# Kernel tuning notes

Measured on AMD Instinct MI355X. Metric: run time of the kernel, lower is better.

The kernel has to match this reference:

```python
import jax, jax.numpy as jnp
import numpy as np

N = 200000; B = 4; C3D = 64; C2D = 128; H = 96; W = 312; MID = 128; OUT = 128
EPS = 1e-5


def _bn(x, g, b):
    # BatchNorm1d in training mode: batch stats over point dim, biased var
    m = x.mean(0, keepdims=True)
    v = x.var(0, keepdims=True)
    return (x - m) * jax.lax.rsqrt(v + EPS) * g + b


def setup_inputs() -> dict:
    key = jax.random.key(0)
    ks = jax.random.split(key, 16)
    bidx = jnp.sort(jax.random.randint(ks[0], (N,), 0, B))  # sorted batch ids (matches per-batch concat order)
    z = jax.random.randint(ks[1], (N,), 0, 40)
    y = jax.random.randint(ks[2], (N,), 0, 1600)
    x = jax.random.randint(ks[3], (N,), 0, 1408)
    voxel_coords = jnp.stack([bidx, z, y, x], 1).astype(jnp.int32)
    voxel_features = jax.random.normal(ks[4], (N, C3D), jnp.float32)
    image_features = jax.random.normal(ks[5], (B, C2D, H, W), jnp.float32)
    base = np.array([[180.0, 0.0, W / 2.0, 0.0],
                     [0.0, 180.0, H / 2.0, 0.0],
                     [0.0, 0.0, 1.0, 0.0]], np.float32)
    P2 = jnp.asarray(base)[None] + 0.01 * jax.random.normal(ks[6], (B, 3, 4), jnp.float32)
    s = 0.05
    params = {
        'vt_w1': s * jax.random.normal(ks[7], (MID, C3D), jnp.float32),
        'vt_b1': jnp.zeros((MID,), jnp.float32),
        'bn1_g': jnp.ones((MID,), jnp.float32),
        'bn1_b': jnp.zeros((MID,), jnp.float32),
        'vt_w2': s * jax.random.normal(ks[8], (MID, MID), jnp.float32),
        'vt_b2': jnp.zeros((MID,), jnp.float32),
        'att_w1': s * jax.random.normal(ks[9], (MID, 2 * MID), jnp.float32),
        'att_b1': jnp.zeros((MID,), jnp.float32),
        'att_w2': s * jax.random.normal(ks[10], (1, MID), jnp.float32),
        'att_b2': jnp.zeros((1,), jnp.float32),
        'fus_w': s * jax.random.normal(ks[11], (OUT, 2 * MID), jnp.float32),
        'fus_b': jnp.zeros((OUT,), jnp.float32),
        'bnf_g': jnp.ones((OUT,), jnp.float32),
        'bnf_b': jnp.zeros((OUT,), jnp.float32),
    }
    return {'voxel_features': voxel_features, 'voxel_coords': voxel_coords,
            'image_features': image_features, 'P2': P2, **params}


def _forward(voxel_features, voxel_coords, image_features, P2,
             vt_w1, vt_b1, bn1_g, bn1_b, vt_w2, vt_b2,
             att_w1, att_b1, att_w2, att_b2, fus_w, fus_b, bnf_g, bnf_b):
    # voxel transform: Linear -> BN -> ReLU -> Linear
    h = voxel_features @ vt_w1.T + vt_b1
    h = jax.nn.relu(_bn(h, bn1_g, bn1_b))
    vfeat = h @ vt_w2.T + vt_b2                                  # (N, MID)

    # 3D -> 2D projection (source multiplies [z,y,x] by voxel_size, faithfully kept)
    voxel_size = jnp.array([0.05, 0.05, 0.1], jnp.float32)
    pc_min = jnp.array([0.0, -40.0, -3.0], jnp.float32)
    pts = voxel_coords[:, 1:].astype(jnp.float32) * voxel_size + pc_min  # (N, 3)
    homo = jnp.concatenate([pts, jnp.ones((pts.shape[0], 1), jnp.float32)], 1)
    b = voxel_coords[:, 0]
    cam = jnp.einsum('nd,nkd->nk', homo, P2[b])                  # (N, 3)
    p2d = cam[:, :2] / (cam[:, 2:3] + 1e-8)
    gx = jnp.clip(p2d[:, 0] / W * 2 - 1, -1.0, 1.0)
    gy = jnp.clip(p2d[:, 1] / H * 2 - 1, -1.0, 1.0)

    # bilinear grid_sample, align_corners=False, zero padding
    ix = ((gx + 1) * W - 1) * 0.5
    iy = ((gy + 1) * H - 1) * 0.5
    x0f = jnp.floor(ix); y0f = jnp.floor(iy)
    wx1 = ix - x0f; wy1 = iy - y0f
    x0 = x0f.astype(jnp.int32); y0 = y0f.astype(jnp.int32)

    def corner(yc, xc, w):
        valid = (xc >= 0) & (xc < W) & (yc >= 0) & (yc < H)
        f = image_features[b, :, jnp.clip(yc, 0, H - 1), jnp.clip(xc, 0, W - 1)]  # (N, C2D)
        return f * (w * valid)[:, None]

    ifeat = (corner(y0, x0, (1 - wx1) * (1 - wy1))
             + corner(y0, x0 + 1, wx1 * (1 - wy1))
             + corner(y0 + 1, x0, (1 - wx1) * wy1)
             + corner(y0 + 1, x0 + 1, wx1 * wy1))                # (N, C2D)

    # attention gate + weighted fusion + Conv1d(k=1) -> BN -> ReLU
    comb = jnp.concatenate([vfeat, ifeat], 1)                    # (N, 2*MID)
    a = jax.nn.sigmoid(jax.nn.relu(comb @ att_w1.T + att_b1) @ att_w2.T + att_b2)  # (N, 1)
    fused = jnp.concatenate([vfeat * a, ifeat * (1 - a)], 1)     # (N, 2*MID)
    out = fused @ fus_w.T + fus_b                                # (N, OUT)
    return jax.nn.relu(_bn(out, bnf_g, bnf_b))


def reference(voxel_features, voxel_coords, image_features, P2,
              vt_w1, vt_b1, bn1_g, bn1_b, vt_w2, vt_b2,
              att_w1, att_b1, att_w2, att_b2, fus_w, fus_b, bnf_g, bnf_b):
    return _forward(voxel_features, voxel_coords, image_features, P2,
                    vt_w1, vt_b1, bn1_g, bn1_b, vt_w2, vt_b2,
                    att_w1, att_b1, att_w2, att_b2, fus_w, fus_b, bnf_g, bnf_b)
```

## Files before the change

### kernel.cpp

```cpp
#include <hip/hip_runtime.h>
#include <hip/hip_bf16.h>

#define NPTS 200000
#define BB   4
#define C3D  64
#define C2D  128
#define HH   96
#define WW   312
#define MID  128
#define OUTC 128

#define WB_W1   0
#define WB_W2   8192
#define WB_AW1  24576
#define WB_AW2  57344
#define WB_FW   57472
#define WB_TOTAL 90240

#define FXS 1048576.0f
#define FXI (1.0 / 1048576.0)

#define WS_H0S    45120
#define WS_H0Q    49216
#define WS_SUM64  53440
#define WS_SSQ64  57536
#define ZERO_N    16512
#define WS_DERIV  61632
#define WS_IMG    62144

typedef __attribute__((ext_vector_type(8))) short s16x8;
typedef __attribute__((ext_vector_type(4))) float f32x4;

__device__ __forceinline__ ushort f2bf(float f) {
    unsigned u = __float_as_uint(f);
    unsigned r = (u + 0x7FFFu + ((u >> 16) & 1u)) >> 16;
    return (ushort)r;
}
__device__ __forceinline__ float bf2f(ushort u) {
    return __uint_as_float(((unsigned)u) << 16);
}
__device__ __forceinline__ void atomic_fx(unsigned long long* p, float v) {
    atomicAdd(p, (unsigned long long)(long long)llrintf(v * FXS));
}
__device__ __forceinline__ s16x8 pack_bf8(float4 a, float4 b) {
    s16x8 v;
    v[0] = (short)f2bf(a.x); v[1] = (short)f2bf(a.y);
    v[2] = (short)f2bf(a.z); v[3] = (short)f2bf(a.w);
    v[4] = (short)f2bf(b.x); v[5] = (short)f2bf(b.y);
    v[6] = (short)f2bf(b.z); v[7] = (short)f2bf(b.w);
    return v;
}

__global__ __launch_bounds__(256) void k_transpose(const float* __restrict__ img,
                                                   ushort* __restrict__ img_bf,
                                                   float* __restrict__ stats,
                                                   const float* __restrict__ w1,
                                                   const float* __restrict__ w2,
                                                   const float* __restrict__ aw1,
                                                   const float* __restrict__ aw2,
                                                   const float* __restrict__ fw,
                                                   ushort* __restrict__ wb) {
    __shared__ float tile[32][33];
    int flat = blockIdx.x * 256 + threadIdx.x;
    if (flat < ZERO_N) stats[flat] = 0.f;
    if (flat < WB_TOTAL) {
        float v;
        if      (flat < WB_W2)  v = w1[flat - WB_W1];
        else if (flat < WB_AW1) v = w2[flat - WB_W2];
        else if (flat < WB_AW2) v = aw1[flat - WB_AW1];
        else if (flat < WB_FW)  v = aw2[flat - WB_AW2];
        else                    v = fw[flat - WB_FW];
        wb[flat] = f2bf(v);
    }

    int bid = blockIdx.x;
    int ct = bid & 3;  bid >>= 2;
    int wt = bid % 10; bid /= 10;
    int h  = bid % HH;
    int b  = bid / HH;
    int tx = threadIdx.x & 31, ty = threadIdx.x >> 5;
    int w0 = wt * 32, c0 = ct * 32;

    #pragma unroll
    for (int i = 0; i < 4; i++) {
        int c = c0 + ty + 8 * i;
        int w = w0 + tx;
        float v = 0.f;
        if (w < WW) v = img[((b * C2D + c) * HH + h) * WW + w];
        tile[ty + 8 * i][tx] = v;
    }
    __syncthreads();
    #pragma unroll
    for (int i = 0; i < 4; i++) {
        int w = w0 + ty + 8 * i;
        int c = c0 + tx;
        if (w < WW) img_bf[((b * HH + h) * WW + w) * C2D + c] = f2bf(tile[tx][ty + 8 * i]);
    }
}

#define H0_ROWS   320
#define H0_BLOCKS (NPTS / H0_ROWS)

__global__ __launch_bounds__(256) void k_h0stats(
        const float* __restrict__ x, const ushort* __restrict__ wb,
        unsigned long long* __restrict__ hs64,
        unsigned long long* __restrict__ hq64) {
    __shared__ float red[4][256];
    const ushort* w1b = wb + WB_W1;
    int t = threadIdx.x, lane = t & 63, wv = t >> 6;
    int l15 = lane & 15, lq = lane >> 4;
    float psum[8], pssq[8];
    #pragma unroll
    for (int nt = 0; nt < 8; nt++) { psum[nt] = 0.f; pssq[nt] = 0.f; }

    int r0 = blockIdx.x * H0_ROWS;
    #pragma unroll 1
    for (int ch = 0; ch < 5; ch++) {
        const float* xr = x + (long)(r0 + ch * 64 + wv * 16 + l15) * C3D;
        float4 xa0 = *(const float4*)(xr + lq * 8);
        float4 xa1 = *(const float4*)(xr + lq * 8 + 4);
        float4 xb0 = *(const float4*)(xr + 32 + lq * 8);
        float4 xb1 = *(const float4*)(xr + 32 + lq * 8 + 4);
        s16x8 af0 = pack_bf8(xa0, xa1);
        s16x8 af1 = pack_bf8(xb0, xb1);
        #pragma unroll
        for (int nt = 0; nt < 8; nt++) {
            f32x4 acc = {0.f, 0.f, 0.f, 0.f};
            s16x8 bf0 = *(const s16x8*)(w1b + (nt * 16 + l15) * 64 + lq * 8);
            s16x8 bf1 = *(const s16x8*)(w1b + (nt * 16 + l15) * 64 + 32 + lq * 8);
            acc = __builtin_amdgcn_mfma_f32_16x16x32_bf16(af0, bf0, acc, 0, 0, 0);
            acc = __builtin_amdgcn_mfma_f32_16x16x32_bf16(af1, bf1, acc, 0, 0, 0);
            psum[nt] += acc[0] + acc[1] + acc[2] + acc[3];
            pssq[nt] += acc[0]*acc[0] + acc[1]*acc[1] + acc[2]*acc[2] + acc[3]*acc[3];
        }
    }
    #pragma unroll
    for (int nt = 0; nt < 8; nt++) {
        psum[nt] += __shfl_xor(psum[nt], 16, 64);
        psum[nt] += __shfl_xor(psum[nt], 32, 64);
        pssq[nt] += __shfl_xor(pssq[nt], 16, 64);
        pssq[nt] += __shfl_xor(pssq[nt], 32, 64);
    }
    if (lane < 16) {
        #pragma unroll
        for (int nt = 0; nt < 8; nt++) {
            red[wv][nt * 16 + l15]       = psum[nt];
            red[wv][128 + nt * 16 + l15] = pssq[nt];
        }
    }
    __syncthreads();
    {
        float v = red[0][t] + red[1][t] + red[2][t] + red[3][t];
        int c = t & 127;
        int slot = blockIdx.x & 15;
        if (t < 128) atomic_fx(&hs64[c * 16 + slot], v);
        else         atomic_fx(&hq64[c * 16 + slot], v);
    }
}

__global__ void k_fin1(const unsigned long long* __restrict__ hs64,
                       const unsigned long long* __restrict__ hq64,
                       const float* __restrict__ g, const float* __restrict__ be,
                       float* __restrict__ s, float* __restrict__ sh) {
    int c = threadIdx.x;
    long long si = 0, qi = 0;
    #pragma unroll
    for (int i = 0; i < 16; i++) {
        si += (long long)hs64[c * 16 + i];
        qi += (long long)hq64[c * 16 + i];
    }
    float S = (float)((double)si * FXI);
    float Q = (float)((double)qi * FXI);
    const float invN = 1.f / (float)NPTS;
    float m = S * invN;
    float v = Q * invN - m * m;
    float sc = g[c] * rsqrtf(v + 1e-5f);
    s[c] = sc;
    sh[c] = be[c] - m * sc;
}

__global__ __launch_bounds__(256, 3) void k_main(
    const float* __restrict__ x, const int* __restrict__ coords,
    const ushort* __restrict__ img_bf, const float* __restrict__ P2,
    const ushort* __restrict__ wb,
    const float* __restrict__ bn1s, const float* __restrict__ bn1sh,
    const float* __restrict__ b2, const float* __restrict__ ab1,
    const float* __restrict__ ab2, const float* __restrict__ fb,
    float* __restrict__ out,
    unsigned long long* __restrict__ sum64, unsigned long long* __restrict__ ssq64)
{
    __shared__ __align__(16) char smem[34816];
    ushort* combs  = (ushort*)smem;
    float*  outs   = (float*)smem;
    float*  a_part = (float*)(smem + 33792);

    const ushort* w1b  = wb + WB_W1;
    const ushort* w2b  = wb + WB_W2;
    const ushort* aw1b = wb + WB_AW1;
    const ushort* aw2b = wb + WB_AW2;
    const ushort* fwb  = wb + WB_FW;

    int t = threadIdx.x;
    int n0 = blockIdx.x * 64;
    int lane = t & 63, wv = t >> 6;
    int l15 = lane & 15, lq = lane >> 4;
    int m0 = wv * 16;
    int cb = wv * 32;

    int grow = m0 + (lane >> 2);
    int qc = lane & 3;
    int poff_[4]; float pwgt_[4];
    {
        int4 cd = *(const int4*)(coords + (long)(n0 + grow) * 4);
        int b = cd.x;
        float p0 = (float)cd.y * 0.05f;
        float p1 = (float)cd.z * 0.05f - 40.f;
        float p2 = (float)cd.w * 0.1f - 3.f;
        const float* P = P2 + b * 12;
        float cam0 = P[0] * p0 + P[1] * p1 + P[2]  * p2 + P[3];
        float cam1 = P[4] * p0 + P[5] * p1 + P[6]  * p2 + P[7];
        float cam2 = P[8] * p0 + P[9] * p1 + P[10] * p2 + P[11];
        float d = cam2 + 1e-8f;
        float px = cam0 / d, py = cam1 / d;
        float gx = fminf(fmaxf(px / (float)WW * 2.f - 1.f, -1.f), 1.f);
        float gy = fminf(fmaxf(py / (float)HH * 2.f - 1.f, -1.f), 1.f);
        float ix = ((gx + 1.f) * (float)WW - 1.f) * 0.5f;
        float iy = ((gy + 1.f) * (float)HH - 1.f) * 0.5f;
        float x0f = floorf(ix), y0f = floorf(iy);
        float wx = ix - x0f, wy = iy - y0f;
        int x0 = (int)x0f, y0 = (int)y0f;
        #pragma unroll
        for (int j = 0; j < 4; j++) {
            int xc = x0 + (j & 1), yc = y0 + (j >> 1);
            float wgt = ((j & 1) ? wx : 1.f - wx) * ((j >> 1) ? wy : 1.f - wy);
            bool valid = (xc >= 0) && (xc < WW) && (yc >= 0) && (yc < HH);
            int xcc = min(max(xc, 0), WW - 1), ycc = min(max(yc, 0), HH - 1);
            poff_[j] = ((b * HH + ycc) * WW + xcc) * C2D;
            pwgt_[j] = valid ? wgt : 0.f;
        }
    }

    #pragma unroll
    for (int g = 0; g < 4; g++) {
        float a8[8];
        #pragma unroll
        for (int e = 0; e < 8; e++) a8[e] = 0.f;
        #pragma unroll
        for (int j = 0; j < 4; j++) {
            s16x8 v = *(const s16x8*)(img_bf + poff_[j] + qc * 32 + g * 8);
            float wgt = pwgt_[j];
            #pragma unroll
            for (int e = 0; e < 8; e++)
                a8[e] += wgt * bf2f((ushort)v[e]);
        }
        s16x8 o;
        #pragma unroll
        for (int e = 0; e < 8; e++) o[e] = (short)f2bf(a8[e]);
        *(s16x8*)(combs + grow * 264 + 128 + qc * 32 + g * 8) = o;
    }

    s16x8 af0, af1;
    {
        const float* xr = x + (long)(n0 + m0 + l15) * C3D;
        float4 xa0 = *(const float4*)(xr + lq * 8);
        float4 xa1 = *(const float4*)(xr + lq * 8 + 4);
        float4 xb0 = *(const float4*)(xr + 32 + lq * 8);
        float4 xb1 = *(const float4*)(xr + 32 + lq * 8 + 4);
        af0 = pack_bf8(xa0, xa1);
        af1 = pack_bf8(xb0, xb1);
    }

    #pragma unroll
    for (int nt = 0; nt < 8; nt++) {
        f32x4 acc = {0.f, 0.f, 0.f, 0.f};
        s16x8 bf0 = *(const s16x8*)(w1b + (nt * 16 + l15) * 64 + lq * 8);
        s16x8 bf1 = *(const s16x8*)(w1b + (nt * 16 + l15) * 64 + 32 + lq * 8);
        acc = __builtin_amdgcn_mfma_f32_16x16x32_bf16(af0, bf0, acc, 0, 0, 0);
        acc = __builtin_amdgcn_mfma_f32_16x16x32_bf16(af1, bf1, acc, 0, 0, 0);
        int c = nt * 16 + l15;
        float sc = bn1s[c], shf = bn1sh[c];
        #pragma unroll
        for (int r = 0; r < 4; r++)
            combs[(m0 + lq * 4 + r) * 264 + c] = f2bf(fmaxf(acc[r] * sc + shf, 0.f));
    }
    __syncthreads();

    f32x4 vacc[4][2];
    #pragma unroll
    for (int nt2 = 0; nt2 < 2; nt2++) {
        int c = cb + nt2 * 16 + l15;
        s16x8 wf[4];
        #pragma unroll
        for (int s = 0; s < 4; s++)
            wf[s] = *(const s16x8*)(w2b + c * 128 + s * 32 + lq * 8);
        #pragma unroll
        for (int mt = 0; mt < 4; mt++) {
            s16x8 ah[4];
            #pragma unroll
            for (int s = 0; s < 4; s++)
                ah[s] = *(const s16x8*)(combs + (mt * 16 + l15) * 264 + s * 32 + lq * 8);
            f32x4 acc = {0.f, 0.f, 0.f, 0.f};
            #pragma unroll
            for (int s = 0; s < 4; s++)
                acc = __builtin_amdgcn_mfma_f32_16x16x32_bf16(ah[s], wf[s], acc, 0, 0, 0);
            vacc[mt][nt2] = acc;
        }
    }
    __syncthreads();

    #pragma unroll
    for (int nt2 = 0; nt2 < 2; nt2++) {
        int c = cb + nt2 * 16 + l15;
        float bb = b2[c];
        #pragma unroll
        for (int mt = 0; mt < 4; mt++)
            #pragma unroll
            for (int r = 0; r < 4; r++)
                combs[(mt * 16 + lq * 4 + r) * 264 + c] = f2bf(vacc[mt][nt2][r] + bb);
    }
    __syncthreads();

    float sp[4][4];
    #pragma unroll
    for (int mt = 0; mt < 4; mt++)
        #pragma unroll
        for (int r = 0; r < 4; r++) sp[mt][r] = 0.f;
    #pragma unroll
    for (int nt2 = 0; nt2 < 2; nt2++) {
        int c = cb + nt2 * 16 + l15;
        s16x8 wf[8];
        #pragma unroll
        for (int s = 0; s < 8; s++)
            wf[s] = *(const s16x8*)(aw1b + c * 256 + s * 32 + lq * 8);
        float bb = ab1[c];
        float w2c = bf2f(aw2b[c]);
        #pragma unroll
        for (int mt = 0; mt < 4; mt++) {
            s16x8 afm[8];
            #pragma unroll
            for (int s = 0; s < 8; s++)
                afm[s] = *(const s16x8*)(combs + (mt * 16 + l15) * 264 + s * 32 + lq * 8);
            f32x4 acc = {0.f, 0.f, 0.f, 0.f};
            #pragma unroll
            for (int s = 0; s < 8; s++)
                acc = __builtin_amdgcn_mfma_f32_16x16x32_bf16(afm[s], wf[s], acc, 0, 0, 0);
            #pragma unroll
            for (int r = 0; r < 4; r++)
                sp[mt][r] += fmaxf(acc[r] + bb, 0.f) * w2c;
        }
    }
    #pragma unroll
    for (int d = 1; d < 16; d <<= 1) {
        #pragma unroll
        for (int mt = 0; mt < 4; mt++)
            #pragma unroll
            for (int r = 0; r < 4; r++)
                sp[mt][r] += __shfl_xor(sp[mt][r], d, 64);
    }
    if (l15 == 0) {
        #pragma unroll
        for (int mt = 0; mt < 4; mt++) {
            f32x4 v = {sp[mt][0], sp[mt][1], sp[mt][2], sp[mt][3]};
            *(f32x4*)(a_part + wv * 64 + mt * 16 + lq * 4) = v;
        }
    }
    __syncthreads();

    {
        int row = m0 + l15;
        float s0 = ab2[0] + a_part[row] + a_part[64 + row] + a_part[128 + row]
                 + a_part[192 + row];
        float a = 1.f / (1.f + expf(-s0));
        #pragma unroll
        for (int j = 0; j < 8; j++) {
            int ch = lq * 8 + j;
            float f = (ch < 16) ? a : 1.f - a;
            ushort* p = combs + row * 264 + ch * 8;
            s16x8 v = *(s16x8*)p;
            s16x8 o;
            #pragma unroll
            for (int e = 0; e < 8; e++) o[e] = (short)f2bf(bf2f((ushort)v[e]) * f);
            *(s16x8*)p = o;
        }
    }
    __syncthreads();

    f32x4 facc[4][2];
    #pragma unroll
    for (int nt2 = 0; nt2 < 2; nt2++) {
        int c = cb + nt2 * 16 + l15;
        s16x8 wf[8];
        #pragma unroll
        for (int s = 0; s < 8; s++)
            wf[s] = *(const s16x8*)(fwb + c * 256 + s * 32 + lq * 8);
        #pragma unroll
        for (int mt = 0; mt < 4; mt++) {
            s16x8 afm[8];
            #pragma unroll
            for (int s = 0; s < 8; s++)
                afm[s] = *(const s16x8*)(combs + (mt * 16 + l15) * 264 + s * 32 + lq * 8);
            f32x4 acc = {0.f, 0.f, 0.f, 0.f};
            #pragma unroll
            for (int s = 0; s < 8; s++)
                acc = __builtin_amdgcn_mfma_f32_16x16x32_bf16(afm[s], wf[s], acc, 0, 0, 0);
            facc[mt][nt2] = acc;
        }
    }
    __syncthreads();

    #pragma unroll
    for (int nt2 = 0; nt2 < 2; nt2++) {
        int c = cb + nt2 * 16 + l15;
        float bb = fb[c];
        #pragma unroll
        for (int mt = 0; mt < 4; mt++)
            #pragma unroll
            for (int r = 0; r < 4; r++)
                outs[(mt * 16 + lq * 4 + r) * 132 + c] = facc[mt][nt2][r] + bb;
    }
    __syncthreads();

    {
        float4* og = (float4*)(out + (long)n0 * OUTC);
        #pragma unroll
        for (int i = 0; i < 8; i++) {
            int f4 = t + 256 * i;
            int row = f4 >> 5, c4 = f4 & 31;
            float4 v = *(const float4*)(outs + row * 132 + c4 * 4);
            og[row * 32 + c4] = v;
        }
        int slot = blockIdx.x & 15;
        if (t < 128) {
            float S = 0.f;
            #pragma unroll 8
            for (int row = 0; row < 64; row++) S += outs[row * 132 + t];
            atomic_fx(&sum64[t * 16 + slot], S);
        } else {
            int c = t - 128;
            float Q = 0.f;
            #pragma unroll 8
            for (int row = 0; row < 64; row++) { float v = outs[row * 132 + c]; Q += v * v; }
            atomic_fx(&ssq64[c * 16 + slot], Q);
        }
    }
}

__global__ __launch_bounds__(256) void k_bnf(float* __restrict__ out,
                                             const unsigned long long* __restrict__ sum64,
                                             const unsigned long long* __restrict__ ssq64,
                                             const float* __restrict__ g,
                                             const float* __restrict__ b) {
    __shared__ float s_s[128], s_sh[128];
    int t = threadIdx.x;
    if (t < 128) {
        long long si = 0, qi = 0;
        #pragma unroll
        for (int i = 0; i < 16; i++) {
            si += (long long)sum64[t * 16 + i];
            qi += (long long)ssq64[t * 16 + i];
        }
        float S = (float)((double)si * FXI);
        float Q = (float)((double)qi * FXI);
        const float invN = 1.f / (float)NPTS;
        float m = S * invN;
        float v = Q * invN - m * m;
        float sc = g[t] * rsqrtf(v + 1e-5f);
        s_s[t] = sc;
        s_sh[t] = b[t] - m * sc;
    }
    __syncthreads();

    long i = (long)blockIdx.x * 256 + t;
    float4* p = (float4*)out;
    float4 v = p[i];
    int c4 = (int)(i & 31);
    float4 sv  = *(const float4*)(s_s + c4 * 4);
    float4 shv = *(const float4*)(s_sh + c4 * 4);
    v.x = fmaxf(v.x * sv.x + shv.x, 0.f);
    v.y = fmaxf(v.y * sv.y + shv.y, 0.f);
    v.z = fmaxf(v.z * sv.z + shv.z, 0.f);
    v.w = fmaxf(v.w * sv.w + shv.w, 0.f);
    p[i] = v;
}

extern "C" void kernel_launch(void* const* d_in, const int* in_sizes, int n_in,
                              void* d_out, int out_size, void* d_ws, size_t ws_size,
                              hipStream_t stream) {
    const float* x      = (const float*)d_in[0];
    const int*   coords = (const int*)d_in[1];
    const float* img    = (const float*)d_in[2];
    const float* P2     = (const float*)d_in[3];
    const float* w1     = (const float*)d_in[4];
    const float* b1     = (const float*)d_in[5];
    const float* g1     = (const float*)d_in[6];
    const float* be1    = (const float*)d_in[7];
    const float* w2     = (const float*)d_in[8];
    const float* b2     = (const float*)d_in[9];
    const float* aw1    = (const float*)d_in[10];
    const float* ab1    = (const float*)d_in[11];
    const float* aw2    = (const float*)d_in[12];
    const float* ab2    = (const float*)d_in[13];
    const float* fw     = (const float*)d_in[14];
    const float* fb     = (const float*)d_in[15];
    const float* gf     = (const float*)d_in[16];
    const float* bef    = (const float*)d_in[17];
    float* out = (float*)d_out;
    (void)b1;

    float* wsf = (float*)d_ws;
    ushort* wb = (ushort*)wsf;
    unsigned long long* hs64  = (unsigned long long*)(wsf + WS_H0S);
    unsigned long long* hq64  = (unsigned long long*)(wsf + WS_H0Q);
    unsigned long long* sum64 = (unsigned long long*)(wsf + WS_SUM64);
    unsigned long long* ssq64 = (unsigned long long*)(wsf + WS_SSQ64);
    float* zero_base = wsf + WS_H0S;
    float* s1  = wsf + WS_DERIV;
    float* sh1 = s1 + 128;
    ushort* img_bf = (ushort*)(wsf + WS_IMG);

    k_transpose<<<BB * HH * 10 * 4, 256, 0, stream>>>(img, img_bf, zero_base,
                                                      w1, w2, aw1, aw2, fw, wb);
    k_h0stats<<<H0_BLOCKS, 256, 0, stream>>>(x, wb, hs64, hq64);
    k_fin1<<<1, 128, 0, stream>>>(hs64, hq64, g1, be1, s1, sh1);
    k_main<<<NPTS / 64, 256, 0, stream>>>(x, coords, img_bf, P2, wb, s1, sh1,
                                          b2, ab1, ab2, fb, out, sum64, ssq64);
    k_bnf<<<NPTS * OUTC / 4 / 256, 256, 0, stream>>>(out, sum64, ssq64, gf, bef);
}
```

Baseline: 469.5 us.

## Merge transpose and BN1 stats kernels, fold finalize into main kernel

The image transpose/weight-conversion kernel and the first-layer BN statistics kernel become one launch by splitting the grid by block index. The stats branch converts w1 to bf16 itself from fp32, since it can no longer rely on the converted weights. The one-block finalize kernel is removed: every k_main block recomputes the BN1 scale and shift from the fixed-point accumulators into shared memory. Stats zeroing moves to a memset. This cuts two kernel launches and their serialization, at the cost of redundant per-block finalize work in k_main and an extra barrier.

```diff
diff --git a/kernel.cpp b/kernel.cpp
--- a/kernel.cpp
+++ b/kernel.cpp
@@ -24,8 +24,7 @@
 #define WS_H0Q    49216
 #define WS_SUM64  53440
 #define WS_SSQ64  57536
-#define ZERO_N    16512
-#define WS_DERIV  61632
+#define WS_STATS_END 61632
 #define WS_IMG    62144
 
 typedef __attribute__((ext_vector_type(8))) short s16x8;
@@ -51,18 +50,86 @@
     return v;
 }
 
-__global__ __launch_bounds__(256) void k_transpose(const float* __restrict__ img,
-                                                   ushort* __restrict__ img_bf,
-                                                   float* __restrict__ stats,
-                                                   const float* __restrict__ w1,
-                                                   const float* __restrict__ w2,
-                                                   const float* __restrict__ aw1,
-                                                   const float* __restrict__ aw2,
-                                                   const float* __restrict__ fw,
-                                                   ushort* __restrict__ wb) {
+#define TRANS_BLOCKS (BB * HH * 10 * 4)
+#define H0_ROWS   320
+#define H0_BLOCKS (NPTS / H0_ROWS)
+
+__global__ __launch_bounds__(256, 3) void k_pre(
+        const float* __restrict__ img, ushort* __restrict__ img_bf,
+        const float* __restrict__ w1, const float* __restrict__ w2,
+        const float* __restrict__ aw1, const float* __restrict__ aw2,
+        const float* __restrict__ fw, ushort* __restrict__ wb,
+        const float* __restrict__ x,
+        unsigned long long* __restrict__ hs64,
+        unsigned long long* __restrict__ hq64) {
     __shared__ float tile[32][33];
+    __shared__ float red[4][256];
+
+    if (blockIdx.x >= TRANS_BLOCKS) {
+        int hbid = blockIdx.x - TRANS_BLOCKS;
+        int t = threadIdx.x, lane = t & 63, wv = t >> 6;
+        int l15 = lane & 15, lq = lane >> 4;
+
+        s16x8 wfa[8], wfb[8];
+        #pragma unroll
+        for (int nt = 0; nt < 8; nt++) {
+            const float* wr = w1 + (nt * 16 + l15) * 64;
+            float4 a0 = *(const float4*)(wr + lq * 8);
+            float4 a1 = *(const float4*)(wr + lq * 8 + 4);
+            float4 b0 = *(const float4*)(wr + 32 + lq * 8);
+            float4 b1 = *(const float4*)(wr + 32 + lq * 8 + 4);
+            wfa[nt] = pack_bf8(a0, a1);
+            wfb[nt] = pack_bf8(b0, b1);
+        }
+        float psum[8], pssq[8];
+        #pragma unroll
+        for (int nt = 0; nt < 8; nt++) { psum[nt] = 0.f; pssq[nt] = 0.f; }
+
+        int r0 = hbid * H0_ROWS;
+        #pragma unroll 1
+        for (int ch = 0; ch < 5; ch++) {
+            const float* xr = x + (long)(r0 + ch * 64 + wv * 16 + l15) * C3D;
+            float4 xa0 = *(const float4*)(xr + lq * 8);
+            float4 xa1 = *(const float4*)(xr + lq * 8 + 4);
+            float4 xb0 = *(const float4*)(xr + 32 + lq * 8);
+            float4 xb1 = *(const float4*)(xr + 32 + lq * 8 + 4);
+            s16x8 af0 = pack_bf8(xa0, xa1);
+            s16x8 af1 = pack_bf8(xb0, xb1);
+            #pragma unroll
+            for (int nt = 0; nt < 8; nt++) {
+                f32x4 acc = {0.f, 0.f, 0.f, 0.f};
+                acc = __builtin_amdgcn_mfma_f32_16x16x32_bf16(af0, wfa[nt], acc, 0, 0, 0);
+                acc = __builtin_amdgcn_mfma_f32_16x16x32_bf16(af1, wfb[nt], acc, 0, 0, 0);
+                psum[nt] += acc[0] + acc[1] + acc[2] + acc[3];
+                pssq[nt] += acc[0]*acc[0] + acc[1]*acc[1] + acc[2]*acc[2] + acc[3]*acc[3];
+            }
+        }
+        #pragma unroll
+        for (int nt = 0; nt < 8; nt++) {
+            psum[nt] += __shfl_xor(psum[nt], 16, 64);
+            psum[nt] += __shfl_xor(psum[nt], 32, 64);
+            pssq[nt] += __shfl_xor(pssq[nt], 16, 64);
+            pssq[nt] += __shfl_xor(pssq[nt], 32, 64);
+        }
+        if (lane < 16) {
+            #pragma unroll
+            for (int nt = 0; nt < 8; nt++) {
+                red[wv][nt * 16 + l15]       = psum[nt];
+                red[wv][128 + nt * 16 + l15] = pssq[nt];
+            }
+        }
+        __syncthreads();
+        {
+            float v = red[0][t] + red[1][t] + red[2][t] + red[3][t];
+            int c = t & 127;
+            int slot = hbid & 15;
+            if (t < 128) atomic_fx(&hs64[c * 16 + slot], v);
+            else         atomic_fx(&hq64[c * 16 + slot], v);
+        }
+        return;
+    }
+
     int flat = blockIdx.x * 256 + threadIdx.x;
-    if (flat < ZERO_N) stats[flat] = 0.f;
     if (flat < WB_TOTAL) {
         float v;
         if      (flat < WB_W2)  v = w1[flat - WB_W1];
@@ -98,92 +165,13 @@
     }
 }
 
-#define H0_ROWS   320
-#define H0_BLOCKS (NPTS / H0_ROWS)
-
-__global__ __launch_bounds__(256) void k_h0stats(
-        const float* __restrict__ x, const ushort* __restrict__ wb,
-        unsigned long long* __restrict__ hs64,
-        unsigned long long* __restrict__ hq64) {
-    __shared__ float red[4][256];
-    const ushort* w1b = wb + WB_W1;
-    int t = threadIdx.x, lane = t & 63, wv = t >> 6;
-    int l15 = lane & 15, lq = lane >> 4;
-    float psum[8], pssq[8];
-    #pragma unroll
-    for (int nt = 0; nt < 8; nt++) { psum[nt] = 0.f; pssq[nt] = 0.f; }
-
-    int r0 = blockIdx.x * H0_ROWS;
-    #pragma unroll 1
-    for (int ch = 0; ch < 5; ch++) {
-        const float* xr = x + (long)(r0 + ch * 64 + wv * 16 + l15) * C3D;
-        float4 xa0 = *(const float4*)(xr + lq * 8);
-        float4 xa1 = *(const float4*)(xr + lq * 8 + 4);
-        float4 xb0 = *(const float4*)(xr + 32 + lq * 8);
-        float4 xb1 = *(const float4*)(xr + 32 + lq * 8 + 4);
-        s16x8 af0 = pack_bf8(xa0, xa1);
-        s16x8 af1 = pack_bf8(xb0, xb1);
-        #pragma unroll
-        for (int nt = 0; nt < 8; nt++) {
-            f32x4 acc = {0.f, 0.f, 0.f, 0.f};
-            s16x8 bf0 = *(const s16x8*)(w1b + (nt * 16 + l15) * 64 + lq * 8);
-            s16x8 bf1 = *(const s16x8*)(w1b + (nt * 16 + l15) * 64 + 32 + lq * 8);
-            acc = __builtin_amdgcn_mfma_f32_16x16x32_bf16(af0, bf0, acc, 0, 0, 0);
-            acc = __builtin_amdgcn_mfma_f32_16x16x32_bf16(af1, bf1, acc, 0, 0, 0);
-            psum[nt] += acc[0] + acc[1] + acc[2] + acc[3];
-            pssq[nt] += acc[0]*acc[0] + acc[1]*acc[1] + acc[2]*acc[2] + acc[3]*acc[3];
-        }
-    }
-    #pragma unroll
-    for (int nt = 0; nt < 8; nt++) {
-        psum[nt] += __shfl_xor(psum[nt], 16, 64);
-        psum[nt] += __shfl_xor(psum[nt], 32, 64);
-        pssq[nt] += __shfl_xor(pssq[nt], 16, 64);
-        pssq[nt] += __shfl_xor(pssq[nt], 32, 64);
-    }
-    if (lane < 16) {
-        #pragma unroll
-        for (int nt = 0; nt < 8; nt++) {
-            red[wv][nt * 16 + l15]       = psum[nt];
-            red[wv][128 + nt * 16 + l15] = pssq[nt];
-        }
-    }
-    __syncthreads();
-    {
-        float v = red[0][t] + red[1][t] + red[2][t] + red[3][t];
-        int c = t & 127;
-        int slot = blockIdx.x & 15;
-        if (t < 128) atomic_fx(&hs64[c * 16 + slot], v);
-        else         atomic_fx(&hq64[c * 16 + slot], v);
-    }
-}
-
-__global__ void k_fin1(const unsigned long long* __restrict__ hs64,
-                       const unsigned long long* __restrict__ hq64,
-                       const float* __restrict__ g, const float* __restrict__ be,
-                       float* __restrict__ s, float* __restrict__ sh) {
-    int c = threadIdx.x;
-    long long si = 0, qi = 0;
-    #pragma unroll
-    for (int i = 0; i < 16; i++) {
-        si += (long long)hs64[c * 16 + i];
-        qi += (long long)hq64[c * 16 + i];
-    }
-    float S = (float)((double)si * FXI);
-    float Q = (float)((double)qi * FXI);
-    const float invN = 1.f / (float)NPTS;
-    float m = S * invN;
-    float v = Q * invN - m * m;
-    float sc = g[c] * rsqrtf(v + 1e-5f);
-    s[c] = sc;
-    sh[c] = be[c] - m * sc;
-}
-
 __global__ __launch_bounds__(256, 3) void k_main(
     const float* __restrict__ x, const int* __restrict__ coords,
     const ushort* __restrict__ img_bf, const float* __restrict__ P2,
     const ushort* __restrict__ wb,
-    const float* __restrict__ bn1s, const float* __restrict__ bn1sh,
+    const unsigned long long* __restrict__ hs64,
+    const unsigned long long* __restrict__ hq64,
+    const float* __restrict__ g1, const float* __restrict__ be1,
     const float* __restrict__ b2, const float* __restrict__ ab1,
     const float* __restrict__ ab2, const float* __restrict__ fb,
     float* __restrict__ out,
@@ -193,6 +181,7 @@
     ushort* combs  = (ushort*)smem;
     float*  outs   = (float*)smem;
     float*  a_part = (float*)(smem + 33792);
+    __shared__ float s_bn1s[128], s_bn1sh[128];
 
     const ushort* w1b  = wb + WB_W1;
     const ushort* w2b  = wb + WB_W2;
@@ -206,6 +195,23 @@
     int l15 = lane & 15, lq = lane >> 4;
     int m0 = wv * 16;
     int cb = wv * 32;
+
+    if (t < 128) {
+        long long si = 0, qi = 0;
+        #pragma unroll
+        for (int i = 0; i < 16; i++) {
+            si += (long long)hs64[t * 16 + i];
+            qi += (long long)hq64[t * 16 + i];
+        }
+        float S = (float)((double)si * FXI);
+        float Q = (float)((double)qi * FXI);
+        const float invN = 1.f / (float)NPTS;
+        float m = S * invN;
+        float v = Q * invN - m * m;
+        float sc = g1[t] * rsqrtf(v + 1e-5f);
+        s_bn1s[t] = sc;
+        s_bn1sh[t] = be1[t] - m * sc;
+    }
 
     int grow = m0 + (lane >> 2);
     int qc = lane & 3;
@@ -269,6 +275,7 @@
         af0 = pack_bf8(xa0, xa1);
         af1 = pack_bf8(xb0, xb1);
     }
+    __syncthreads();
 
     #pragma unroll
     for (int nt = 0; nt < 8; nt++) {
@@ -278,7 +285,7 @@
         acc = __builtin_amdgcn_mfma_f32_16x16x32_bf16(af0, bf0, acc, 0, 0, 0);
         acc = __builtin_amdgcn_mfma_f32_16x16x32_bf16(af1, bf1, acc, 0, 0, 0);
         int c = nt * 16 + l15;
-        float sc = bn1s[c], shf = bn1sh[c];
+        float sc = s_bn1s[c], shf = s_bn1sh[c];
         #pragma unroll
         for (int r = 0; r < 4; r++)
             combs[(m0 + lq * 4 + r) * 264 + c] = f2bf(fmaxf(acc[r] * sc + shf, 0.f));
@@ -513,16 +520,14 @@
     unsigned long long* hq64  = (unsigned long long*)(wsf + WS_H0Q);
     unsigned long long* sum64 = (unsigned long long*)(wsf + WS_SUM64);
     unsigned long long* ssq64 = (unsigned long long*)(wsf + WS_SSQ64);
-    float* zero_base = wsf + WS_H0S;
-    float* s1  = wsf + WS_DERIV;
-    float* sh1 = s1 + 128;
     ushort* img_bf = (ushort*)(wsf + WS_IMG);
 
-    k_transpose<<<BB * HH * 10 * 4, 256, 0, stream>>>(img, img_bf, zero_base,
-                                                      w1, w2, aw1, aw2, fw, wb);
-    k_h0stats<<<H0_BLOCKS, 256, 0, stream>>>(x, wb, hs64, hq64);
-    k_fin1<<<1, 128, 0, stream>>>(hs64, hq64, g1, be1, s1, sh1);
-    k_main<<<NPTS / 64, 256, 0, stream>>>(x, coords, img_bf, P2, wb, s1, sh1,
+    hipMemsetAsync(wsf + WS_H0S, 0, (size_t)(WS_STATS_END - WS_H0S) * 4, stream);
+    k_pre<<<TRANS_BLOCKS + H0_BLOCKS, 256, 0, stream>>>(img, img_bf,
+                                                        w1, w2, aw1, aw2, fw, wb,
+                                                        x, hs64, hq64);
+    k_main<<<NPTS / 64, 256, 0, stream>>>(x, coords, img_bf, P2, wb,
+                                          hs64, hq64, g1, be1,
                                           b2, ab1, ab2, fb, out, sum64, ssq64);
     k_bnf<<<NPTS * OUTC / 4 / 256, 256, 0, stream>>>(out, sum64, ssq64, gf, bef);
 }
```

Measured after the change: 509.5 us. +8.5%, slower.
